# Kernel tuning notes

Measured on AMD Instinct MI355X. Metric: run time of the kernel, lower is better.

The kernel has to match this reference:

```python
import jax, jax.numpy as jnp
import numpy as np

B, S, E = 2, 2048, 1024
H, D = 16, 64


def setup_inputs() -> dict:
    key = jax.random.key(0)
    ks = jax.random.split(key, 9)
    s_in = 1.0 / np.sqrt(E)
    s_out = 1.0 / np.sqrt(H * D)
    return {
        "x": jax.random.normal(ks[0], (B, S, E), dtype=jnp.float32),
        "W_q": jax.random.uniform(ks[1], (H, E, D), jnp.float32, -s_in, s_in),
        "b_q": jax.random.uniform(ks[2], (H, D), jnp.float32, -s_in, s_in),
        "W_k": jax.random.uniform(ks[3], (H, E, D), jnp.float32, -s_in, s_in),
        "b_k": jax.random.uniform(ks[4], (H, D), jnp.float32, -s_in, s_in),
        "W_v": jax.random.uniform(ks[5], (H, E, D), jnp.float32, -s_in, s_in),
        "b_v": jax.random.uniform(ks[6], (H, D), jnp.float32, -s_in, s_in),
        "W_o": jax.random.uniform(ks[7], (H * D, E), jnp.float32, -s_out, s_out),
        "b_o": jax.random.uniform(ks[8], (E,), jnp.float32, -s_out, s_out),
    }


def reference(x, W_q, b_q, W_k, b_k, W_v, b_v, W_o, b_o):
    # batched per-head projections: [B,S,E] x [H,E,D] -> [B,H,S,D]
    q = jnp.einsum("bse,hed->bhsd", x, W_q) + b_q[None, :, None, :]
    k = jnp.einsum("bse,hed->bhsd", x, W_k) + b_k[None, :, None, :]
    v = jnp.einsum("bse,hed->bhsd", x, W_v) + b_v[None, :, None, :]
    scale = 1.0 / jnp.sqrt(jnp.asarray(D, dtype=x.dtype))
    score = jnp.einsum("bhsd,bhtd->bhst", q, k) * scale  # [B,H,S,S]
    causal = jnp.tril(jnp.ones((S, S), dtype=bool))
    score = jnp.where(causal[None, None], score, -jnp.inf)
    w = jax.nn.softmax(score, axis=-1)
    o = jnp.einsum("bhst,bhtd->bhsd", w, v)  # [B,H,S,D]
    # concat heads along last dim (head-major order matches torch.cat)
    o = o.transpose(0, 2, 1, 3).reshape(B, S, H * D)
    # dropout is identity in eval mode
    return o @ W_o + b_o
```

## Files before the change

kernel.cpp:

```cpp
#include <hip/hip_runtime.h>


typedef __attribute__((ext_vector_type(8)))  __bf16 bf16x8;
typedef __attribute__((ext_vector_type(4)))  __bf16 bf16x4;
typedef __attribute__((ext_vector_type(2)))  __bf16 bf16x2;
typedef __attribute__((ext_vector_type(4)))  float  f32x4;
typedef __attribute__((ext_vector_type(16))) float  f32x16;
typedef __attribute__((ext_vector_type(2)))  unsigned int u32x2;
typedef __attribute__((ext_vector_type(4)))  unsigned int u32x4;

#define LOG2E 1.4426950408889634f
#define SM_SC (0.125f * LOG2E)

static __device__ __forceinline__ void gl2lds16(const void* g, void* l) {
    __builtin_amdgcn_global_load_lds(
        (__attribute__((address_space(1))) void*)(void*)g,
        (__attribute__((address_space(3))) void*)l, 16, 0, 0);
}

static __device__ __forceinline__ unsigned pku(float a, float b) {
    bf16x2 t = { (__bf16)a, (__bf16)b };
    return __builtin_bit_cast(unsigned, t);
}

__global__ void __launch_bounds__(256)
prep_all_kern(const float* __restrict__ x, const float* __restrict__ Wq,
              const float* __restrict__ Wk, const float* __restrict__ Wv,
              const float* __restrict__ bq, const float* __restrict__ bk,
              const float* __restrict__ bv, const float* __restrict__ Wo,
              __bf16* __restrict__ xb, __bf16* __restrict__ wt,
              float* __restrict__ bias, __bf16* __restrict__ wto) {
    __shared__ float T[64][65];
    const int t = threadIdx.x;
    const int bx = blockIdx.x;
    if (bx < 4096) {
        int i = (bx * 256 + t) * 4;
        f32x4 v = *(const f32x4*)(x + i);
        bf16x4 o = { (__bf16)v[0], (__bf16)v[1], (__bf16)v[2], (__bf16)v[3] };
        *(bf16x4*)(xb + i) = o;
    } else if (bx < 4864) {
        const int blk = bx - 4096;
        const int kt = blk & 15, ph = blk >> 4;
        const int h = ph & 15, p = ph >> 4;
        const float* W  = (p == 0) ? Wq : (p == 1) ? Wk : Wv;
        const float* bb = (p == 0) ? bq : (p == 1) ? bk : bv;
        #pragma unroll
        for (int i = 0; i < 4; ++i) {
            int flat = i * 1024 + t * 4;
            int kr = flat >> 6, d4 = flat & 63;
            f32x4 v = *(const f32x4*)(W + (h << 16) + ((kt * 64 + kr) << 6) + d4);
            T[kr][d4] = v[0]; T[kr][d4 + 1] = v[1]; T[kr][d4 + 2] = v[2]; T[kr][d4 + 3] = v[3];
        }
        __syncthreads();
        const int d = t >> 2, kq = (t & 3) << 4;
        bf16x8 o0, o1;
        #pragma unroll
        for (int j = 0; j < 8; ++j) o0[j] = (__bf16)T[kq + j][d];
        #pragma unroll
        for (int j = 0; j < 8; ++j) o1[j] = (__bf16)T[kq + 8 + j][d];
        __bf16* dst = wt + (((size_t)(p * 1024 + h * 64 + d)) << 10) + kt * 64 + kq;
        *(bf16x8*)dst = o0;
        *(bf16x8*)(dst + 8) = o1;
        if (kt == 0 && t < 64) bias[p * 1024 + h * 64 + t] = bb[h * 64 + t];
    } else {
        const int blk = bx - 4864;
        const int nt = blk & 15, ktile = blk >> 4;
        #pragma unroll
        for (int i = 0; i < 4; ++i) {
            int flat = i * 1024 + t * 4;
            int kr = flat >> 6, n4 = flat & 63;
            f32x4 v = *(const f32x4*)(Wo + ((size_t)(ktile * 64 + kr) << 10) + nt * 64 + n4);
            T[kr][n4] = v[0]; T[kr][n4 + 1] = v[1]; T[kr][n4 + 2] = v[2]; T[kr][n4 + 3] = v[3];
        }
        __syncthreads();
        const int n = t >> 2, kq = (t & 3) << 4;
        bf16x8 o0, o1;
        #pragma unroll
        for (int j = 0; j < 8; ++j) o0[j] = (__bf16)T[kq + j][n];
        #pragma unroll
        for (int j = 0; j < 8; ++j) o1[j] = (__bf16)T[kq + 8 + j][n];
        __bf16* dst = wto + (((size_t)(nt * 64 + n)) << 10) + ktile * 64 + kq;
        *(bf16x8*)dst = o0;
        *(bf16x8*)(dst + 8) = o1;
    }
}

template <int EPI>
__global__ void __launch_bounds__(256, 2)
gemm_bt(const __bf16* __restrict__ A, const __bf16* __restrict__ Bt,
        const float* __restrict__ bias,
        __bf16* __restrict__ outq, __bf16* __restrict__ outk, __bf16* __restrict__ outv,
        float* __restrict__ outf)
{
    __shared__ __align__(16) __bf16 As[128 * 64];
    __shared__ __align__(16) __bf16 Bs[128 * 64];
    const int tid = threadIdx.x;
    const int wid = tid >> 6, lane = tid & 63;
    const int r = lane & 15, g = lane >> 4;
    const int m0 = blockIdx.y << 7, n0 = blockIdx.x << 7;
    const int wr = wid >> 1, wc = wid & 1;
    f32x4 acc[4][4] = {};
    for (int k0 = 0; k0 < 1024; k0 += 64) {
        #pragma unroll
        for (int c = 0; c < 4; ++c) {
            int cq = (c * 4 + wid) * 64 + lane;
            int row = cq >> 3, ci = cq & 7;
            gl2lds16(A  + (((size_t)(m0 + row)) << 10) + k0 + ci * 8, As + (c * 4 + wid) * 512);
            gl2lds16(Bt + (((size_t)(n0 + row)) << 10) + k0 + ci * 8, Bs + (c * 4 + wid) * 512);
        }
        __syncthreads();
        bf16x8 af[2][4], bfr[2][4];
        #pragma unroll
        for (int kh = 0; kh < 2; ++kh)
            #pragma unroll
            for (int i = 0; i < 4; ++i) {
                af[kh][i]  = *(const bf16x8*)&As[(wr * 64 + i * 16 + r) * 64 + kh * 32 + g * 8];
                bfr[kh][i] = *(const bf16x8*)&Bs[(wc * 64 + i * 16 + r) * 64 + kh * 32 + g * 8];
            }
        #pragma unroll
        for (int kh = 0; kh < 2; ++kh)
            #pragma unroll
            for (int mi = 0; mi < 4; ++mi)
                #pragma unroll
                for (int ni = 0; ni < 4; ++ni)
                    acc[mi][ni] = __builtin_amdgcn_mfma_f32_16x16x32_bf16(
                        af[kh][mi], bfr[kh][ni], acc[mi][ni], 0, 0, 0);
        __syncthreads();
    }
    if (EPI == 0) {
        #pragma unroll
        for (int ni = 0; ni < 4; ++ni) {
            int n = n0 + wc * 64 + ni * 16 + r;
            float bv = bias[n];
            int p = n >> 10, rem = n & 1023, h = rem >> 6, d = rem & 63;
            #pragma unroll
            for (int mi = 0; mi < 4; ++mi) {
                int mb = m0 + wr * 64 + mi * 16 + g * 4;
                int b = mb >> 11, s = mb & 2047;
                f32x4 v = acc[mi][ni];
                if (p < 2) {
                    __bf16* dst = (p == 0) ? outq : outk;
                    size_t base = (((size_t)(b * 16 + h)) * 2048 + s) * 64 + d;
                    #pragma unroll
                    for (int j = 0; j < 4; ++j)
                        dst[base + (size_t)j * 64] = (__bf16)(v[j] + bv);
                } else {
                    bf16x4 pk = { (__bf16)(v[0] + bv), (__bf16)(v[1] + bv),
                                  (__bf16)(v[2] + bv), (__bf16)(v[3] + bv) };
                    *(bf16x4*)&outv[(((size_t)(b * 16 + h)) * 64 + d) * 2048 + s] = pk;
                }
            }
        }
    } else {
        #pragma unroll
        for (int ni = 0; ni < 4; ++ni) {
            int n = n0 + wc * 64 + ni * 16 + r;
            float bv = bias[n];
            #pragma unroll
            for (int mi = 0; mi < 4; ++mi) {
                int mb = m0 + wr * 64 + mi * 16 + g * 4;
                f32x4 v = acc[mi][ni];
                #pragma unroll
                for (int j = 0; j < 4; ++j)
                    outf[((size_t)(mb + j) << 10) + n] = v[j] + bv;
            }
        }
    }
}

__global__ void __launch_bounds__(256, 3)
attn_kern(const __bf16* __restrict__ q, const __bf16* __restrict__ k,
          const __bf16* __restrict__ vT, __bf16* __restrict__ pO0,
          __bf16* __restrict__ pO1, float* __restrict__ ml)
{
    __shared__ __align__(16) __bf16 Ks [2][64][72];
    __shared__ __align__(16) __bf16 VsT[2][64][72];
    const int tid = threadIdx.x, lane = tid & 63, w = tid >> 6;
    const int r31 = lane & 31, hi = lane >> 5;
    const int bid = blockIdx.x;
    const int rnk = bid >> 5, bh = bid & 31;
    const int j = 15 - (rnk >> 1), kvh = rnk & 1;
    const int b = bh >> 4, h = bh & 15;
    const __bf16* qh  = q  + ((size_t)bh << 17);
    const __bf16* khp = k  + ((size_t)bh << 17);
    const __bf16* vhp = vT + ((size_t)bh << 17);
    __bf16* pO = kvh ? pO1 : pO0;
    const int srow = tid >> 3, sci = tid & 7;

    const int qb0 = j << 7;
    const int wrow0 = qb0 + w * 32;
    const int mg = wrow0 + r31;
    const int tbeg = kvh * (j + 1), tend = tbeg + (j + 1);

    bf16x8 qf[4];
    #pragma unroll
    for (int kk = 0; kk < 4; ++kk)
        qf[kk] = *(const bf16x8*)&qh[(size_t)mg * 64 + kk * 16 + hi * 8];

    f32x16 oacc[2] = {};
    f32x16 lacc = {};
    float mrun = -3.0e38f;
    bf16x8 onesf;
    #pragma unroll
    for (int jj = 0; jj < 8; ++jj) onesf[jj] = (__bf16)1.0f;

    #pragma unroll
    for (int it = 0; it < 2; ++it) {
        int row = srow + it * 32;
        *(bf16x8*)&Ks [0][row][sci * 8] = *(const bf16x8*)&khp[(size_t)(tbeg * 64 + row) * 64 + sci * 8];
        *(bf16x8*)&VsT[0][row][sci * 8] = *(const bf16x8*)&vhp[(size_t)row * 2048 + tbeg * 64 + sci * 8];
    }
    __syncthreads();

    for (int t = tbeg; t < tend; ++t) {
        const int cur = (t - tbeg) & 1, nxt = cur ^ 1;
        const int n0 = t << 6;
        const bool pre = (t + 1 < tend);
        bf16x8 nk[2], nv[2];
        if (pre) {
            int n1 = n0 + 64;
            #pragma unroll
            for (int it = 0; it < 2; ++it) {
                int row = srow + it * 32;
                nk[it] = *(const bf16x8*)&khp[(size_t)(n1 + row) * 64 + sci * 8];
                nv[it] = *(const bf16x8*)&vhp[(size_t)row * 2048 + n1 + sci * 8];
            }
        }
        if (n0 <= wrow0 + 31) {
            f32x16 sacc[2] = {};
            #pragma unroll
            for (int kk = 0; kk < 4; ++kk) {
                bf16x8 kf0 = *(const bf16x8*)&Ks[cur][r31]     [kk * 16 + hi * 8];
                bf16x8 kf1 = *(const bf16x8*)&Ks[cur][32 + r31][kk * 16 + hi * 8];
                sacc[0] = __builtin_amdgcn_mfma_f32_32x32x16_bf16(kf0, qf[kk], sacc[0], 0, 0, 0);
                sacc[1] = __builtin_amdgcn_mfma_f32_32x32x16_bf16(kf1, qf[kk], sacc[1], 0, 0, 0);
            }
            if (n0 + 63 > wrow0) {
                #pragma unroll
                for (int nf = 0; nf < 2; ++nf)
                    #pragma unroll
                    for (int i = 0; i < 16; ++i) {
                        int n = n0 + nf * 32 + (i & 3) + 8 * (i >> 2) + 4 * hi;
                        if (n > mg) sacc[nf][i] = -3.0e38f;
                    }
            }
            float mx[16];
            #pragma unroll
            for (int i = 0; i < 16; ++i) mx[i] = fmaxf(sacc[0][i], sacc[1][i]);
            #pragma unroll
            for (int s = 8; s > 0; s >>= 1)
                #pragma unroll
                for (int i = 0; i < 8; ++i)
                    if (i < s) mx[i] = fmaxf(mx[i], mx[i + s]);
            float pmh = mx[0];
            if (!__all((pmh - mrun) * SM_SC <= 8.0f)) {
                float pm = fmaxf(pmh, __shfl_xor(pmh, 32));
                float mnew = fmaxf(mrun, pm);
                float fac = exp2f((mrun - mnew) * SM_SC);
                lacc[0] *= fac;
                #pragma unroll
                for (int df = 0; df < 2; ++df)
                    #pragma unroll
                    for (int i = 0; i < 16; ++i) oacc[df][i] *= fac;
                mrun = mnew;
            }
            #pragma unroll
            for (int nf = 0; nf < 2; ++nf)
                #pragma unroll
                for (int i = 0; i < 16; ++i)
                    sacc[nf][i] = exp2f((sacc[nf][i] - mrun) * SM_SC);
            #pragma unroll
            for (int nf = 0; nf < 2; ++nf) {
                unsigned pk[8];
                #pragma unroll
                for (int jj = 0; jj < 8; ++jj)
                    pk[jj] = pku(sacc[nf][2 * jj], sacc[nf][2 * jj + 1]);
#if __has_builtin(__builtin_amdgcn_permlane32_swap)
                u32x2 s02 = __builtin_amdgcn_permlane32_swap(pk[0], pk[2], false, false);
                u32x2 s13 = __builtin_amdgcn_permlane32_swap(pk[1], pk[3], false, false);
                u32x2 s46 = __builtin_amdgcn_permlane32_swap(pk[4], pk[6], false, false);
                u32x2 s57 = __builtin_amdgcn_permlane32_swap(pk[5], pk[7], false, false);
                u32x4 fw0 = { s02[0], s13[0], s02[1], s13[1] };
                u32x4 fw1 = { s46[0], s57[0], s46[1], s57[1] };
#else
                unsigned rxa = __shfl_xor(hi ? pk[0] : pk[2], 32);
                unsigned rxb = __shfl_xor(hi ? pk[1] : pk[3], 32);
                unsigned rxc = __shfl_xor(hi ? pk[4] : pk[6], 32);
                unsigned rxd = __shfl_xor(hi ? pk[5] : pk[7], 32);
                u32x4 fw0 = { hi ? rxa : pk[0], hi ? rxb : pk[1],
                              hi ? pk[2] : rxa, hi ? pk[3] : rxb };
                u32x4 fw1 = { hi ? rxc : pk[4], hi ? rxd : pk[5],
                              hi ? pk[6] : rxc, hi ? pk[7] : rxd };
#endif
                bf16x8 pf0 = __builtin_bit_cast(bf16x8, fw0);
                bf16x8 pf1 = __builtin_bit_cast(bf16x8, fw1);
                #pragma unroll
                for (int kl = 0; kl < 2; ++kl) {
                    const bf16x8 pf = kl ? pf1 : pf0;
                    const int kk = nf * 2 + kl;
                    bf16x8 af0 = *(const bf16x8*)&VsT[cur][r31]     [kk * 16 + hi * 8];
                    bf16x8 af1 = *(const bf16x8*)&VsT[cur][32 + r31][kk * 16 + hi * 8];
                    oacc[0] = __builtin_amdgcn_mfma_f32_32x32x16_bf16(af0, pf, oacc[0], 0, 0, 0);
                    oacc[1] = __builtin_amdgcn_mfma_f32_32x32x16_bf16(af1, pf, oacc[1], 0, 0, 0);
                    lacc    = __builtin_amdgcn_mfma_f32_32x32x16_bf16(onesf, pf, lacc, 0, 0, 0);
                }
            }
        }
        if (pre) {
            #pragma unroll
            for (int it = 0; it < 2; ++it) {
                int row = srow + it * 32;
                *(bf16x8*)&Ks [nxt][row][sci * 8] = nk[it];
                *(bf16x8*)&VsT[nxt][row][sci * 8] = nv[it];
            }
        }
        __syncthreads();
    }
    float lrun = lacc[0];
    float inv = (lrun > 0.f) ? 1.0f / lrun : 0.f;
    #pragma unroll
    for (int df = 0; df < 2; ++df)
        #pragma unroll
        for (int td = 0; td < 8; ++td) {
            bf16x2 pr = { (__bf16)(oacc[df][2 * td] * inv),
                          (__bf16)(oacc[df][2 * td + 1] * inv) };
            int d = df * 32 + 8 * (td >> 1) + 4 * hi + 2 * (td & 1);
            *(bf16x2*)&pO[((size_t)(b * 2048 + mg) << 10) + h * 64 + d] = pr;
        }
    if (hi == 0) {
        size_t mi = (((size_t)kvh * 32 + bh) * 2048 + mg) * 2;
        ml[mi] = mrun;
        ml[mi + 1] = lrun;
    }
}

__global__ void merge_kern(const __bf16* __restrict__ pO0, const float* __restrict__ ml,
                           __bf16* __restrict__ ob)
{
    int i = blockIdx.x * 256 + threadIdx.x;
    int m = i >> 7, rem = i & 127, h = rem >> 3, d8 = (rem & 7) * 8;
    int bh = (m >> 11) * 16 + h, sr = m & 2047;
    size_t i0 = ((size_t)bh * 2048 + sr) * 2;
    float m0 = ml[i0], l0 = ml[i0 + 1];
    float m1 = ml[131072 + i0], l1 = ml[131072 + i0 + 1];
    float mx = fmaxf(m0, m1);
    float c0 = exp2f((m0 - mx) * SM_SC) * l0;
    float c1 = exp2f((m1 - mx) * SM_SC) * l1;
    float inv = 1.0f / (c0 + c1);
    float w0 = c0 * inv, w1 = c1 * inv;
    size_t off = (size_t)m * 1024 + h * 64 + d8;
    bf16x8 a = *(const bf16x8*)(pO0 + off);
    bf16x8 c = *(const bf16x8*)(ob + off);
    bf16x8 r;
    #pragma unroll
    for (int j = 0; j < 8; ++j) r[j] = (__bf16)(w0 * (float)a[j] + w1 * (float)c[j]);
    *(bf16x8*)(ob + off) = r;
}

extern "C" void kernel_launch(void* const* d_in, const int* in_sizes, int n_in,
                              void* d_out, int out_size, void* d_ws, size_t ws_size,
                              hipStream_t stream) {
    const float* x  = (const float*)d_in[0];
    const float* Wq = (const float*)d_in[1];
    const float* bq = (const float*)d_in[2];
    const float* Wk = (const float*)d_in[3];
    const float* bk = (const float*)d_in[4];
    const float* Wv = (const float*)d_in[5];
    const float* bv = (const float*)d_in[6];
    const float* Wo = (const float*)d_in[7];
    const float* bo = (const float*)d_in[8];
    float* out = (float*)d_out;
    char* ws = (char*)d_ws;
    __bf16* xb    = (__bf16*)(ws + 0);
    __bf16* wtqkv = (__bf16*)(ws + 8388608);
    __bf16* wot   = (__bf16*)(ws + 14680064);
    float*  biasq = (float*) (ws + 16777216);
    __bf16* qb    = (__bf16*)(ws + 16793600);
    __bf16* kb    = (__bf16*)(ws + 25182208);
    __bf16* vtb   = (__bf16*)(ws + 33570816);
    __bf16* ob    = (__bf16*)(ws + 41959424);
    __bf16* pO0   = xb;
    float*  mlbuf = (float*)(ws + 8388608);

    prep_all_kern<<<5120, 256, 0, stream>>>(x, Wq, Wk, Wv, bq, bk, bv, Wo,
                                            xb, wtqkv, biasq, wot);
    gemm_bt<0><<<dim3(24, 32), 256, 0, stream>>>(xb, wtqkv, biasq, qb, kb, vtb, nullptr);
    attn_kern<<<1024, 256, 0, stream>>>(qb, kb, vtb, pO0, ob, mlbuf);
    merge_kern<<<4096, 256, 0, stream>>>(pO0, mlbuf, ob);
    gemm_bt<1><<<dim3(8, 32), 256, 0, stream>>>(ob, wot, bo, nullptr, nullptr, nullptr, out);
}
```

Before: 123.0 us.

## Split causal attention KV range four ways and merge four partials

The attention kernel now splits each query block's causal KV tiles across four blocks instead of two, doubling the grid so more work runs concurrently and per-block KV loops get shorter. Blocks whose share is empty skip the loop. The merge kernel combines four partial outputs using their running max and sum. The two extra partial buffers live in the output buffer as scratch. The QKV/out GEMM launch bounds also rise from two to three blocks per CU. In exchange, the merge reads and writes more partial traffic, and the tighter launch bounds may add register spills in the GEMM.

```diff
diff --git a/kernel.cpp b/kernel.cpp
--- a/kernel.cpp
+++ b/kernel.cpp
@@ -86,7 +86,7 @@
 }
 
 template <int EPI>
-__global__ void __launch_bounds__(256, 2)
+__global__ void __launch_bounds__(256, 3)
 gemm_bt(const __bf16* __restrict__ A, const __bf16* __restrict__ Bt,
         const float* __restrict__ bias,
         __bf16* __restrict__ outq, __bf16* __restrict__ outk, __bf16* __restrict__ outv,
@@ -171,7 +171,8 @@
 __global__ void __launch_bounds__(256, 3)
 attn_kern(const __bf16* __restrict__ q, const __bf16* __restrict__ k,
           const __bf16* __restrict__ vT, __bf16* __restrict__ pO0,
-          __bf16* __restrict__ pO1, float* __restrict__ ml)
+          __bf16* __restrict__ pO1, __bf16* __restrict__ pO2,
+          __bf16* __restrict__ pO3, float* __restrict__ ml)
 {
     __shared__ __align__(16) __bf16 Ks [2][64][72];
     __shared__ __align__(16) __bf16 VsT[2][64][72];
@@ -179,142 +180,148 @@
     const int r31 = lane & 31, hi = lane >> 5;
     const int bid = blockIdx.x;
     const int rnk = bid >> 5, bh = bid & 31;
-    const int j = 15 - (rnk >> 1), kvh = rnk & 1;
+    const int j = 15 - (rnk >> 2), kvq = rnk & 3;
     const int b = bh >> 4, h = bh & 15;
     const __bf16* qh  = q  + ((size_t)bh << 17);
     const __bf16* khp = k  + ((size_t)bh << 17);
     const __bf16* vhp = vT + ((size_t)bh << 17);
-    __bf16* pO = kvh ? pO1 : pO0;
+    __bf16* pO = (kvq == 0) ? pO0 : (kvq == 1) ? pO1 : (kvq == 2) ? pO2 : pO3;
     const int srow = tid >> 3, sci = tid & 7;
 
     const int qb0 = j << 7;
     const int wrow0 = qb0 + w * 32;
     const int mg = wrow0 + r31;
-    const int tbeg = kvh * (j + 1), tend = tbeg + (j + 1);
-
-    bf16x8 qf[4];
-    #pragma unroll
-    for (int kk = 0; kk < 4; ++kk)
-        qf[kk] = *(const bf16x8*)&qh[(size_t)mg * 64 + kk * 16 + hi * 8];
+    const int c2 = 2 * (j + 1);
+    const int base = c2 >> 2, rem = c2 & 3;
+    const int len = base + (kvq < rem ? 1 : 0);
+    const int tbeg = kvq * base + min(kvq, rem);
+    const int tend = tbeg + len;
 
     f32x16 oacc[2] = {};
     f32x16 lacc = {};
     float mrun = -3.0e38f;
-    bf16x8 onesf;
-    #pragma unroll
-    for (int jj = 0; jj < 8; ++jj) onesf[jj] = (__bf16)1.0f;
-
-    #pragma unroll
-    for (int it = 0; it < 2; ++it) {
-        int row = srow + it * 32;
-        *(bf16x8*)&Ks [0][row][sci * 8] = *(const bf16x8*)&khp[(size_t)(tbeg * 64 + row) * 64 + sci * 8];
-        *(bf16x8*)&VsT[0][row][sci * 8] = *(const bf16x8*)&vhp[(size_t)row * 2048 + tbeg * 64 + sci * 8];
-    }
-    __syncthreads();
-
-    for (int t = tbeg; t < tend; ++t) {
-        const int cur = (t - tbeg) & 1, nxt = cur ^ 1;
-        const int n0 = t << 6;
-        const bool pre = (t + 1 < tend);
-        bf16x8 nk[2], nv[2];
-        if (pre) {
-            int n1 = n0 + 64;
-            #pragma unroll
-            for (int it = 0; it < 2; ++it) {
-                int row = srow + it * 32;
-                nk[it] = *(const bf16x8*)&khp[(size_t)(n1 + row) * 64 + sci * 8];
-                nv[it] = *(const bf16x8*)&vhp[(size_t)row * 2048 + n1 + sci * 8];
-            }
-        }
-        if (n0 <= wrow0 + 31) {
-            f32x16 sacc[2] = {};
-            #pragma unroll
-            for (int kk = 0; kk < 4; ++kk) {
-                bf16x8 kf0 = *(const bf16x8*)&Ks[cur][r31]     [kk * 16 + hi * 8];
-                bf16x8 kf1 = *(const bf16x8*)&Ks[cur][32 + r31][kk * 16 + hi * 8];
-                sacc[0] = __builtin_amdgcn_mfma_f32_32x32x16_bf16(kf0, qf[kk], sacc[0], 0, 0, 0);
-                sacc[1] = __builtin_amdgcn_mfma_f32_32x32x16_bf16(kf1, qf[kk], sacc[1], 0, 0, 0);
-            }
-            if (n0 + 63 > wrow0) {
+
+    if (len > 0) {
+        bf16x8 qf[4];
+        #pragma unroll
+        for (int kk = 0; kk < 4; ++kk)
+            qf[kk] = *(const bf16x8*)&qh[(size_t)mg * 64 + kk * 16 + hi * 8];
+        bf16x8 onesf;
+        #pragma unroll
+        for (int jj = 0; jj < 8; ++jj) onesf[jj] = (__bf16)1.0f;
+
+        #pragma unroll
+        for (int it = 0; it < 2; ++it) {
+            int row = srow + it * 32;
+            *(bf16x8*)&Ks [0][row][sci * 8] = *(const bf16x8*)&khp[(size_t)(tbeg * 64 + row) * 64 + sci * 8];
+            *(bf16x8*)&VsT[0][row][sci * 8] = *(const bf16x8*)&vhp[(size_t)row * 2048 + tbeg * 64 + sci * 8];
+        }
+        __syncthreads();
+
+        for (int t = tbeg; t < tend; ++t) {
+            const int cur = (t - tbeg) & 1, nxt = cur ^ 1;
+            const int n0 = t << 6;
+            const bool pre = (t + 1 < tend);
+            bf16x8 nk[2], nv[2];
+            if (pre) {
+                int n1 = n0 + 64;
+                #pragma unroll
+                for (int it = 0; it < 2; ++it) {
+                    int row = srow + it * 32;
+                    nk[it] = *(const bf16x8*)&khp[(size_t)(n1 + row) * 64 + sci * 8];
+                    nv[it] = *(const bf16x8*)&vhp[(size_t)row * 2048 + n1 + sci * 8];
+                }
+            }
+            if (n0 <= wrow0 + 31) {
+                f32x16 sacc[2] = {};
+                #pragma unroll
+                for (int kk = 0; kk < 4; ++kk) {
+                    bf16x8 kf0 = *(const bf16x8*)&Ks[cur][r31]     [kk * 16 + hi * 8];
+                    bf16x8 kf1 = *(const bf16x8*)&Ks[cur][32 + r31][kk * 16 + hi * 8];
+                    sacc[0] = __builtin_amdgcn_mfma_f32_32x32x16_bf16(kf0, qf[kk], sacc[0], 0, 0, 0);
+                    sacc[1] = __builtin_amdgcn_mfma_f32_32x32x16_bf16(kf1, qf[kk], sacc[1], 0, 0, 0);
+                }
+                if (n0 + 63 > wrow0) {
+                    #pragma unroll
+                    for (int nf = 0; nf < 2; ++nf)
+                        #pragma unroll
+                        for (int i = 0; i < 16; ++i) {
+                            int n = n0 + nf * 32 + (i & 3) + 8 * (i >> 2) + 4 * hi;
+                            if (n > mg) sacc[nf][i] = -3.0e38f;
+                        }
+                }
+                float mx[16];
+                #pragma unroll
+                for (int i = 0; i < 16; ++i) mx[i] = fmaxf(sacc[0][i], sacc[1][i]);
+                #pragma unroll
+                for (int s = 8; s > 0; s >>= 1)
+                    #pragma unroll
+                    for (int i = 0; i < 8; ++i)
+                        if (i < s) mx[i] = fmaxf(mx[i], mx[i + s]);
+                float pmh = mx[0];
+                if (!__all((pmh - mrun) * SM_SC <= 8.0f)) {
+                    float pm = fmaxf(pmh, __shfl_xor(pmh, 32));
+                    float mnew = fmaxf(mrun, pm);
+                    float fac = exp2f((mrun - mnew) * SM_SC);
+                    lacc[0] *= fac;
+                    #pragma unroll
+                    for (int df = 0; df < 2; ++df)
+                        #pragma unroll
+                        for (int i = 0; i < 16; ++i) oacc[df][i] *= fac;
+                    mrun = mnew;
+                }
                 #pragma unroll
                 for (int nf = 0; nf < 2; ++nf)
                     #pragma unroll
-                    for (int i = 0; i < 16; ++i) {
-                        int n = n0 + nf * 32 + (i & 3) + 8 * (i >> 2) + 4 * hi;
-                        if (n > mg) sacc[nf][i] = -3.0e38f;
+                    for (int i = 0; i < 16; ++i)
+                        sacc[nf][i] = exp2f((sacc[nf][i] - mrun) * SM_SC);
+                #pragma unroll
+                for (int nf = 0; nf < 2; ++nf) {
+                    unsigned pk[8];
+                    #pragma unroll
+                    for (int jj = 0; jj < 8; ++jj)
+                        pk[jj] = pku(sacc[nf][2 * jj], sacc[nf][2 * jj + 1]);
+#if __has_builtin(__builtin_amdgcn_permlane32_swap)
+                    u32x2 s02 = __builtin_amdgcn_permlane32_swap(pk[0], pk[2], false, false);
+                    u32x2 s13 = __builtin_amdgcn_permlane32_swap(pk[1], pk[3], false, false);
+                    u32x2 s46 = __builtin_amdgcn_permlane32_swap(pk[4], pk[6], false, false);
+                    u32x2 s57 = __builtin_amdgcn_permlane32_swap(pk[5], pk[7], false, false);
+                    u32x4 fw0 = { s02[0], s13[0], s02[1], s13[1] };
+                    u32x4 fw1 = { s46[0], s57[0], s46[1], s57[1] };
+#else
+                    unsigned rxa = __shfl_xor(hi ? pk[0] : pk[2], 32);
+                    unsigned rxb = __shfl_xor(hi ? pk[1] : pk[3], 32);
+                    unsigned rxc = __shfl_xor(hi ? pk[4] : pk[6], 32);
+                    unsigned rxd = __shfl_xor(hi ? pk[5] : pk[7], 32);
+                    u32x4 fw0 = { hi ? rxa : pk[0], hi ? rxb : pk[1],
+                                  hi ? pk[2] : rxa, hi ? pk[3] : rxb };
+                    u32x4 fw1 = { hi ? rxc : pk[4], hi ? rxd : pk[5],
+                                  hi ? pk[6] : rxc, hi ? pk[7] : rxd };
+#endif
+                    bf16x8 pf0 = __builtin_bit_cast(bf16x8, fw0);
+                    bf16x8 pf1 = __builtin_bit_cast(bf16x8, fw1);
+                    #pragma unroll
+                    for (int kl = 0; kl < 2; ++kl) {
+                        const bf16x8 pf = kl ? pf1 : pf0;
+                        const int kk = nf * 2 + kl;
+                        bf16x8 af0 = *(const bf16x8*)&VsT[cur][r31]     [kk * 16 + hi * 8];
+                        bf16x8 af1 = *(const bf16x8*)&VsT[cur][32 + r31][kk * 16 + hi * 8];
+                        oacc[0] = __builtin_amdgcn_mfma_f32_32x32x16_bf16(af0, pf, oacc[0], 0, 0, 0);
+                        oacc[1] = __builtin_amdgcn_mfma_f32_32x32x16_bf16(af1, pf, oacc[1], 0, 0, 0);
+                        lacc    = __builtin_amdgcn_mfma_f32_32x32x16_bf16(onesf, pf, lacc, 0, 0, 0);
                     }
-            }
-            float mx[16];
-            #pragma unroll
-            for (int i = 0; i < 16; ++i) mx[i] = fmaxf(sacc[0][i], sacc[1][i]);
-            #pragma unroll
-            for (int s = 8; s > 0; s >>= 1)
-                #pragma unroll
-                for (int i = 0; i < 8; ++i)
-                    if (i < s) mx[i] = fmaxf(mx[i], mx[i + s]);
-            float pmh = mx[0];
-            if (!__all((pmh - mrun) * SM_SC <= 8.0f)) {
-                float pm = fmaxf(pmh, __shfl_xor(pmh, 32));
-                float mnew = fmaxf(mrun, pm);
-                float fac = exp2f((mrun - mnew) * SM_SC);
-                lacc[0] *= fac;
-                #pragma unroll
-                for (int df = 0; df < 2; ++df)
-                    #pragma unroll
-                    for (int i = 0; i < 16; ++i) oacc[df][i] *= fac;
-                mrun = mnew;
-            }
-            #pragma unroll
-            for (int nf = 0; nf < 2; ++nf)
-                #pragma unroll
-                for (int i = 0; i < 16; ++i)
-                    sacc[nf][i] = exp2f((sacc[nf][i] - mrun) * SM_SC);
-            #pragma unroll
-            for (int nf = 0; nf < 2; ++nf) {
-                unsigned pk[8];
-                #pragma unroll
-                for (int jj = 0; jj < 8; ++jj)
-                    pk[jj] = pku(sacc[nf][2 * jj], sacc[nf][2 * jj + 1]);
-#if __has_builtin(__builtin_amdgcn_permlane32_swap)
-                u32x2 s02 = __builtin_amdgcn_permlane32_swap(pk[0], pk[2], false, false);
-                u32x2 s13 = __builtin_amdgcn_permlane32_swap(pk[1], pk[3], false, false);
-                u32x2 s46 = __builtin_amdgcn_permlane32_swap(pk[4], pk[6], false, false);
-                u32x2 s57 = __builtin_amdgcn_permlane32_swap(pk[5], pk[7], false, false);
-                u32x4 fw0 = { s02[0], s13[0], s02[1], s13[1] };
-                u32x4 fw1 = { s46[0], s57[0], s46[1], s57[1] };
-#else
-                unsigned rxa = __shfl_xor(hi ? pk[0] : pk[2], 32);
-                unsigned rxb = __shfl_xor(hi ? pk[1] : pk[3], 32);
-                unsigned rxc = __shfl_xor(hi ? pk[4] : pk[6], 32);
-                unsigned rxd = __shfl_xor(hi ? pk[5] : pk[7], 32);
-                u32x4 fw0 = { hi ? rxa : pk[0], hi ? rxb : pk[1],
-                              hi ? pk[2] : rxa, hi ? pk[3] : rxb };
-                u32x4 fw1 = { hi ? rxc : pk[4], hi ? rxd : pk[5],
-                              hi ? pk[6] : rxc, hi ? pk[7] : rxd };
-#endif
-                bf16x8 pf0 = __builtin_bit_cast(bf16x8, fw0);
-                bf16x8 pf1 = __builtin_bit_cast(bf16x8, fw1);
-                #pragma unroll
-                for (int kl = 0; kl < 2; ++kl) {
-                    const bf16x8 pf = kl ? pf1 : pf0;
-                    const int kk = nf * 2 + kl;
-                    bf16x8 af0 = *(const bf16x8*)&VsT[cur][r31]     [kk * 16 + hi * 8];
-                    bf16x8 af1 = *(const bf16x8*)&VsT[cur][32 + r31][kk * 16 + hi * 8];
-                    oacc[0] = __builtin_amdgcn_mfma_f32_32x32x16_bf16(af0, pf, oacc[0], 0, 0, 0);
-                    oacc[1] = __builtin_amdgcn_mfma_f32_32x32x16_bf16(af1, pf, oacc[1], 0, 0, 0);
-                    lacc    = __builtin_amdgcn_mfma_f32_32x32x16_bf16(onesf, pf, lacc, 0, 0, 0);
-                }
-            }
-        }
-        if (pre) {
-            #pragma unroll
-            for (int it = 0; it < 2; ++it) {
-                int row = srow + it * 32;
-                *(bf16x8*)&Ks [nxt][row][sci * 8] = nk[it];
-                *(bf16x8*)&VsT[nxt][row][sci * 8] = nv[it];
-            }
-        }
-        __syncthreads();
+                }
+            }
+            if (pre) {
+                #pragma unroll
+                for (int it = 0; it < 2; ++it) {
+                    int row = srow + it * 32;
+                    *(bf16x8*)&Ks [nxt][row][sci * 8] = nk[it];
+                    *(bf16x8*)&VsT[nxt][row][sci * 8] = nv[it];
+                }
+            }
+            __syncthreads();
+        }
     }
     float lrun = lacc[0];
     float inv = (lrun > 0.f) ? 1.0f / lrun : 0.f;
@@ -328,32 +335,40 @@
             *(bf16x2*)&pO[((size_t)(b * 2048 + mg) << 10) + h * 64 + d] = pr;
         }
     if (hi == 0) {
-        size_t mi = (((size_t)kvh * 32 + bh) * 2048 + mg) * 2;
+        size_t mi = (((size_t)kvq * 32 + bh) * 2048 + mg) * 2;
         ml[mi] = mrun;
         ml[mi + 1] = lrun;
     }
 }
 
-__global__ void merge_kern(const __bf16* __restrict__ pO0, const float* __restrict__ ml,
+__global__ void merge_kern(const __bf16* __restrict__ pO0, const __bf16* __restrict__ pO2,
+                           const __bf16* __restrict__ pO3, const float* __restrict__ ml,
                            __bf16* __restrict__ ob)
 {
     int i = blockIdx.x * 256 + threadIdx.x;
     int m = i >> 7, rem = i & 127, h = rem >> 3, d8 = (rem & 7) * 8;
     int bh = (m >> 11) * 16 + h, sr = m & 2047;
     size_t i0 = ((size_t)bh * 2048 + sr) * 2;
-    float m0 = ml[i0], l0 = ml[i0 + 1];
-    float m1 = ml[131072 + i0], l1 = ml[131072 + i0 + 1];
-    float mx = fmaxf(m0, m1);
-    float c0 = exp2f((m0 - mx) * SM_SC) * l0;
-    float c1 = exp2f((m1 - mx) * SM_SC) * l1;
-    float inv = 1.0f / (c0 + c1);
-    float w0 = c0 * inv, w1 = c1 * inv;
+    float mm0 = ml[i0],          ll0 = ml[i0 + 1];
+    float mm1 = ml[131072 + i0], ll1 = ml[131072 + i0 + 1];
+    float mm2 = ml[262144 + i0], ll2 = ml[262144 + i0 + 1];
+    float mm3 = ml[393216 + i0], ll3 = ml[393216 + i0 + 1];
+    float mx = fmaxf(fmaxf(mm0, mm1), fmaxf(mm2, mm3));
+    float c0 = exp2f((mm0 - mx) * SM_SC) * ll0;
+    float c1 = exp2f((mm1 - mx) * SM_SC) * ll1;
+    float c2 = exp2f((mm2 - mx) * SM_SC) * ll2;
+    float c3 = exp2f((mm3 - mx) * SM_SC) * ll3;
+    float inv = 1.0f / (c0 + c1 + c2 + c3);
     size_t off = (size_t)m * 1024 + h * 64 + d8;
-    bf16x8 a = *(const bf16x8*)(pO0 + off);
-    bf16x8 c = *(const bf16x8*)(ob + off);
+    bf16x8 a0 = *(const bf16x8*)(pO0 + off);
+    bf16x8 a1 = *(const bf16x8*)(ob + off);
+    bf16x8 a2 = *(const bf16x8*)(pO2 + off);
+    bf16x8 a3 = *(const bf16x8*)(pO3 + off);
     bf16x8 r;
     #pragma unroll
-    for (int j = 0; j < 8; ++j) r[j] = (__bf16)(w0 * (float)a[j] + w1 * (float)c[j]);
+    for (int j = 0; j < 8; ++j)
+        r[j] = (__bf16)((c0 * (float)a0[j] + c1 * (float)a1[j] +
+                         c2 * (float)a2[j] + c3 * (float)a3[j]) * inv);
     *(bf16x8*)(ob + off) = r;
 }
 
@@ -380,12 +395,14 @@
     __bf16* vtb   = (__bf16*)(ws + 33570816);
     __bf16* ob    = (__bf16*)(ws + 41959424);
     __bf16* pO0   = xb;
+    __bf16* pO2   = (__bf16*)d_out;
+    __bf16* pO3   = (__bf16*)d_out + 4194304;
     float*  mlbuf = (float*)(ws + 8388608);
 
     prep_all_kern<<<5120, 256, 0, stream>>>(x, Wq, Wk, Wv, bq, bk, bv, Wo,
                                             xb, wtqkv, biasq, wot);
     gemm_bt<0><<<dim3(24, 32), 256, 0, stream>>>(xb, wtqkv, biasq, qb, kb, vtb, nullptr);
-    attn_kern<<<1024, 256, 0, stream>>>(qb, kb, vtb, pO0, ob, mlbuf);
-    merge_kern<<<4096, 256, 0, stream>>>(pO0, mlbuf, ob);
+    attn_kern<<<2048, 256, 0, stream>>>(qb, kb, vtb, pO0, ob, pO2, pO3, mlbuf);
+    merge_kern<<<2048, 256, 0, stream>>>(pO0, pO2, pO3, mlbuf, ob);
     gemm_bt<1><<<dim3(8, 32), 256, 0, stream>>>(ob, wot, bo, nullptr, nullptr, nullptr, out);
 }
```

Result: no change. 122.6 us (-0.3%).
